# Performance work log

Measured on AMD Instinct MI355X. Metric: run time of the kernel, lower is better.

The kernel has to match this reference:

```python
import jax, jax.numpy as jnp
import numpy as np

N = 100000   # nodes
E = 1600000  # edges
G = 1000     # graphs in batch
F = 16       # in_features
D = 128      # embed_dim
C = 100      # num_centroid
K = 2        # num_class
L = 3        # num_layers


def setup_inputs() -> dict:
    key = jax.random.key(0)
    ks = jax.random.split(key, 8)
    x = jax.random.normal(ks[0], (N, F), dtype=jnp.float32)
    edge_index = jax.random.randint(ks[1], (2, E), 0, N)
    batch = jnp.sort(jax.random.randint(ks[2], (N,), 0, G))
    # learned params (xavier-like scaled, per init code)
    W_embed = jax.random.normal(ks[3], (D, F), dtype=jnp.float32) * 0.1
    W_convs = jax.random.normal(ks[4], (L, D, D), dtype=jnp.float32) * 0.05
    centroids = jax.random.normal(ks[5], (C, D), dtype=jnp.float32) * 0.1
    W_out = jax.random.normal(ks[6], (K, C), dtype=jnp.float32) * 0.1
    b_out = jax.random.uniform(ks[7], (K,), jnp.float32, -1e-4, 1e-4)
    return {"x": x, "edge_index": edge_index, "batch": batch,
            "W_embed": W_embed, "W_convs": W_convs, "centroids": centroids,
            "W_out": W_out, "b_out": b_out}


def _gcn_conv(h, W, src, dst, deg_isqrt):
    # h: [N, D]; standard GCNConv with self-loops, no bias
    m = h @ W.T                                   # [N, D]
    coef = deg_isqrt[src] * deg_isqrt[dst]        # [E+N]
    msg = m[src] * coef[:, None]                  # gather + scale
    return jax.ops.segment_sum(msg, dst, num_segments=N)


def reference(x, edge_index, batch, W_embed, W_convs, centroids, W_out, b_out):
    src0, dst0 = edge_index[0], edge_index[1]
    loop = jnp.arange(N, dtype=src0.dtype)
    src = jnp.concatenate([src0, loop])           # A + I edges
    dst = jnp.concatenate([dst0, loop])
    deg = jax.ops.segment_sum(jnp.ones(src.shape[0], jnp.float32), dst, num_segments=N)
    deg_isqrt = jax.lax.rsqrt(jnp.maximum(deg, 1.0))

    h = x @ W_embed.T                             # embedding, no bias
    for i in range(L):
        h = _gcn_conv(h, W_convs[i], src, dst, deg_isqrt)
        h = jax.nn.relu(h)                        # manifold (Euclidean) nonlinearity

    # centroid Euclidean distances: [N, C] via ||a-b||^2 = |a|^2 + |b|^2 - 2ab
    x2 = jnp.sum(h * h, axis=1, keepdims=True)            # [N,1]
    c2 = jnp.sum(centroids * centroids, axis=1)[None, :]  # [1,C]
    d2 = jnp.maximum(x2 + c2 - 2.0 * (h @ centroids.T), 0.0)
    dist = jnp.sqrt(d2 + 1e-12)                            # [N,C]

    # mean-pool per graph
    sums = jax.ops.segment_sum(dist, batch, num_segments=G)           # [G,C]
    cnts = jax.ops.segment_sum(jnp.ones((N,), jnp.float32), batch, num_segments=G)
    pooled = sums / jnp.maximum(cnts, 1.0)[:, None]

    return pooled @ W_out.T + b_out               # [G, K]
```

## Files before the change

### kernel.cpp

```cpp
#include <hip/hip_runtime.h>
#include <hip/hip_bf16.h>
#include <hip/hip_fp16.h>

constexpr int N_ = 100000;
constexpr int E_ = 1600000;
constexpr int G_ = 1000;
constexpr int D_ = 128;
constexpr int C_ = 100;
constexpr int K_ = 2;
constexpr int L_ = 3;
constexpr int NSB = (N_ + 255) / 256;
constexpr int NR_ = 8;
constexpr int RN_ = (N_ + NR_ - 1) / NR_;
constexpr int EPB_ = 1280;
constexpr int NCH_ = (E_ + EPB_ - 1) / EPB_;

using f16x8 = __attribute__((ext_vector_type(8))) _Float16;
using f16x4 = __attribute__((ext_vector_type(4))) _Float16;
using f32x4 = __attribute__((ext_vector_type(4))) float;

__global__ __launch_bounds__(256) void count_deg_xcd(
    const int* __restrict__ dstv, int* __restrict__ deg) {
    int r = blockIdx.x & 7;
    int chunk = blockIdx.x >> 3;
    int lo = r * RN_;
    int hi = lo + RN_;
    int ebeg = chunk * EPB_;
    int eend = ebeg + EPB_; if (eend > E_) eend = E_;
    for (int e = ebeg + threadIdx.x; e < eend; e += 256) {
        int d = dstv[e];
        if (d >= lo && d < hi) atomicAdd(&deg[d], 1);
    }
}

__global__ void scan_block_sums(const int* __restrict__ deg, int* __restrict__ bsums,
                                float* __restrict__ dis) {
    __shared__ int sh[256];
    int i = blockIdx.x * 256 + threadIdx.x;
    int v = (i < N_) ? deg[i] : 0;
    if (i < N_) dis[i] = 1.0f / sqrtf((float)(v + 1));
    sh[threadIdx.x] = v;
    __syncthreads();
    for (int off = 128; off > 0; off >>= 1) {
        if (threadIdx.x < off) sh[threadIdx.x] += sh[threadIdx.x + off];
        __syncthreads();
    }
    if (threadIdx.x == 0) bsums[blockIdx.x] = sh[0];
}

__global__ void scan_offsets(int* __restrict__ bsums, int nb) {
    __shared__ int a[512], b[512];
    int t = threadIdx.x;
    int v = (t < nb) ? bsums[t] : 0;
    a[t] = v;
    __syncthreads();
    int* src = a; int* dst = b;
    for (int off = 1; off < 512; off <<= 1) {
        int x = src[t] + ((t >= off) ? src[t - off] : 0);
        dst[t] = x;
        __syncthreads();
        int* tmp = src; src = dst; dst = tmp;
    }
    if (t < nb) bsums[t] = src[t] - v;
}

__global__ void scan_write(const int* __restrict__ deg, const int* __restrict__ boffs,
                           int* __restrict__ rowp) {
    __shared__ int a[256], b[256];
    int t = threadIdx.x;
    int i = blockIdx.x * 256 + t;
    int v = (i < N_) ? deg[i] : 0;
    a[t] = v;
    __syncthreads();
    int* src = a; int* dst = b;
    for (int off = 1; off < 256; off <<= 1) {
        int x = src[t] + ((t >= off) ? src[t - off] : 0);
        dst[t] = x;
        __syncthreads();
        int* tmp = src; src = dst; dst = tmp;
    }
    if (i < N_) rowp[i] = boffs[blockIdx.x] + src[t] - v;
    if (i == 0) rowp[N_] = E_;
}

__global__ __launch_bounds__(256) void fill_csr_xcd(
    const int* __restrict__ srcv, const int* __restrict__ dstv,
    const int* __restrict__ rowp, int* __restrict__ cursor,
    int* __restrict__ csr) {
    int r = blockIdx.x & 7;
    int chunk = blockIdx.x >> 3;
    int lo = r * RN_;
    int hi = lo + RN_;
    int ebeg = chunk * EPB_;
    int eend = ebeg + EPB_; if (eend > E_) eend = E_;
    for (int e = ebeg + threadIdx.x; e < eend; e += 256) {
        int d = dstv[e];
        if (d >= lo && d < hi) {
            int pos = atomicAdd(&cursor[d], 1);
            csr[rowp[d] + pos] = srcv[e];
        }
    }
}

__global__ __launch_bounds__(128) void embed_kernel(
    const float* __restrict__ x, const float* __restrict__ Wemb,
    _Float16* __restrict__ h) {
    __shared__ float4 xs[64 * 4];
    int t = threadIdx.x;
    float w[16];
#pragma unroll
    for (int f = 0; f < 16; ++f) w[f] = Wemb[t * 16 + f];
    int n0 = blockIdx.x * 64;
    const float4* x4 = (const float4*)x;
    for (int idx = t; idx < 64 * 4; idx += 128) {
        int gi = n0 * 4 + idx;
        xs[idx] = (gi < N_ * 4) ? x4[gi] : make_float4(0.f, 0.f, 0.f, 0.f);
    }
    __syncthreads();
    int lim = min(64, N_ - n0);
    for (int j = 0; j < lim; ++j) {
        float4 x0 = xs[j * 4 + 0], x1 = xs[j * 4 + 1];
        float4 x2 = xs[j * 4 + 2], x3 = xs[j * 4 + 3];
        float acc = x0.x * w[0] + x0.y * w[1] + x0.z * w[2] + x0.w * w[3]
                  + x1.x * w[4] + x1.y * w[5] + x1.z * w[6] + x1.w * w[7]
                  + x2.x * w[8] + x2.y * w[9] + x2.z * w[10] + x2.w * w[11]
                  + x3.x * w[12] + x3.y * w[13] + x3.z * w[14] + x3.w * w[15];
        h[(size_t)(n0 + j) * 128 + t] = (_Float16)acc;
    }
}

template<int FP16OUT>
__global__ __launch_bounds__(256) void mfma_gemm(
    const _Float16* __restrict__ h, const float* __restrict__ W,
    void* __restrict__ outp, int ncols, const float* __restrict__ dis) {
    int t = threadIdx.x;
    int w = t >> 6;
    int l = t & 63;
    int l15 = l & 15;
    int g = l >> 4;
    int nb0 = blockIdx.x * 128;

    f16x8 afr[2][4];
#pragma unroll
    for (int cg = 0; cg < 2; ++cg) {
        int c = 16 * w + 64 * cg + l15;
#pragma unroll
        for (int ks = 0; ks < 4; ++ks) {
            f16x8 af = {0, 0, 0, 0, 0, 0, 0, 0};
            if (c < ncols) {
                const float* wp = &W[c * 128 + 32 * ks + 8 * g];
                float4 w0 = *(const float4*)wp;
                float4 w1 = *(const float4*)(wp + 4);
                af[0] = (_Float16)w0.x; af[1] = (_Float16)w0.y;
                af[2] = (_Float16)w0.z; af[3] = (_Float16)w0.w;
                af[4] = (_Float16)w1.x; af[5] = (_Float16)w1.y;
                af[6] = (_Float16)w1.z; af[7] = (_Float16)w1.w;
            }
            afr[cg][ks] = af;
        }
    }

    for (int nt = 0; nt < 8; ++nt) {
        int nb = nb0 + 16 * nt;
        int node = nb + l15;
        int nodeL = node < N_ ? node : 0;
        f16x8 bfr[4];
#pragma unroll
        for (int ks = 0; ks < 4; ++ks)
            bfr[ks] = *(const f16x8*)&h[(size_t)nodeL * 128 + 32 * ks + 8 * g];
        f32x4 acc0 = {0.f, 0.f, 0.f, 0.f};
        f32x4 acc1 = {0.f, 0.f, 0.f, 0.f};
#pragma unroll
        for (int ks = 0; ks < 4; ++ks) {
            acc0 = __builtin_amdgcn_mfma_f32_16x16x32_f16(afr[0][ks], bfr[ks], acc0, 0, 0, 0);
            acc1 = __builtin_amdgcn_mfma_f32_16x16x32_f16(afr[1][ks], bfr[ks], acc1, 0, 0, 0);
        }
        if (node < N_) {
            int cb = 16 * w + 4 * g;
            if (FP16OUT) {
                float s = dis[node];
                ushort* mh = (ushort*)outp;
                __half2 p01 = __float22half2_rn(make_float2(acc0[0] * s, acc0[1] * s));
                __half2 p23 = __float22half2_rn(make_float2(acc0[2] * s, acc0[3] * s));
                uint2 u0;
                u0.x = *(unsigned int*)&p01; u0.y = *(unsigned int*)&p23;
                *(uint2*)&mh[(size_t)node * 128 + cb] = u0;
                __half2 q01 = __float22half2_rn(make_float2(acc1[0] * s, acc1[1] * s));
                __half2 q23 = __float22half2_rn(make_float2(acc1[2] * s, acc1[3] * s));
                uint2 u1;
                u1.x = *(unsigned int*)&q01; u1.y = *(unsigned int*)&q23;
                *(uint2*)&mh[(size_t)node * 128 + cb + 64] = u1;
            } else {
                float* o = (float*)outp;
                *(float4*)&o[(size_t)node * 128 + cb] =
                    make_float4(acc0[0], acc0[1], acc0[2], acc0[3]);
                *(float4*)&o[(size_t)node * 128 + cb + 64] =
                    make_float4(acc1[0], acc1[1], acc1[2], acc1[3]);
            }
        }
    }
}

__device__ inline float4 h4f4(uint2 u) {
    float2 fa = __half22float2(*(__half2*)&u.x);
    float2 fb = __half22float2(*(__half2*)&u.y);
    return make_float4(fa.x, fa.y, fb.x, fb.y);
}

__global__ __launch_bounds__(256) void aggregate(
    const ushort* __restrict__ mh, _Float16* __restrict__ hout,
    const int* __restrict__ rowp, const int* __restrict__ csr,
    const float* __restrict__ dis, float* __restrict__ x2out) {
    int t = threadIdx.x;
    int lane = t & 63;
    int l32 = lane & 31;
    int hbase = lane & 32;
    int node = blockIdx.x * 8 + ((t >> 6) << 1) + (hbase >> 5);
    const uint2* m2 = (const uint2*)mh;

    float4 acc0 = h4f4(m2[(size_t)node * 32 + l32]);
    float4 acc1 = make_float4(0.f, 0.f, 0.f, 0.f);
    int beg = rowp[node], end = rowp[node + 1];
    for (int base = beg; base < end; base += 32) {
        int cnt = end - base; if (cnt > 32) cnt = 32;
        int myidx = (l32 < cnt) ? csr[base + l32] : 0;
        int j = 0;
        for (; j + 8 <= cnt; j += 8) {
            int s0 = __shfl(myidx, hbase + j);
            int s1 = __shfl(myidx, hbase + j + 1);
            int s2 = __shfl(myidx, hbase + j + 2);
            int s3 = __shfl(myidx, hbase + j + 3);
            int s4 = __shfl(myidx, hbase + j + 4);
            int s5 = __shfl(myidx, hbase + j + 5);
            int s6 = __shfl(myidx, hbase + j + 6);
            int s7 = __shfl(myidx, hbase + j + 7);
            uint2 u0 = m2[(size_t)s0 * 32 + l32];
            uint2 u1 = m2[(size_t)s1 * 32 + l32];
            uint2 u2 = m2[(size_t)s2 * 32 + l32];
            uint2 u3 = m2[(size_t)s3 * 32 + l32];
            uint2 u4 = m2[(size_t)s4 * 32 + l32];
            uint2 u5 = m2[(size_t)s5 * 32 + l32];
            uint2 u6 = m2[(size_t)s6 * 32 + l32];
            uint2 u7 = m2[(size_t)s7 * 32 + l32];
            float4 v0 = h4f4(u0), v1 = h4f4(u1), v2 = h4f4(u2), v3 = h4f4(u3);
            float4 v4 = h4f4(u4), v5 = h4f4(u5), v6 = h4f4(u6), v7 = h4f4(u7);
            acc0.x += (v0.x + v1.x) + (v2.x + v3.x);
            acc0.y += (v0.y + v1.y) + (v2.y + v3.y);
            acc0.z += (v0.z + v1.z) + (v2.z + v3.z);
            acc0.w += (v0.w + v1.w) + (v2.w + v3.w);
            acc1.x += (v4.x + v5.x) + (v6.x + v7.x);
            acc1.y += (v4.y + v5.y) + (v6.y + v7.y);
            acc1.z += (v4.z + v5.z) + (v6.z + v7.z);
            acc1.w += (v4.w + v5.w) + (v6.w + v7.w);
        }
        for (; j + 4 <= cnt; j += 4) {
            int s0 = __shfl(myidx, hbase + j);
            int s1 = __shfl(myidx, hbase + j + 1);
            int s2 = __shfl(myidx, hbase + j + 2);
            int s3 = __shfl(myidx, hbase + j + 3);
            uint2 u0 = m2[(size_t)s0 * 32 + l32];
            uint2 u1 = m2[(size_t)s1 * 32 + l32];
            uint2 u2 = m2[(size_t)s2 * 32 + l32];
            uint2 u3 = m2[(size_t)s3 * 32 + l32];
            float4 v0 = h4f4(u0), v1 = h4f4(u1), v2 = h4f4(u2), v3 = h4f4(u3);
            acc0.x += (v0.x + v1.x) + (v2.x + v3.x);
            acc0.y += (v0.y + v1.y) + (v2.y + v3.y);
            acc0.z += (v0.z + v1.z) + (v2.z + v3.z);
            acc0.w += (v0.w + v1.w) + (v2.w + v3.w);
        }
        for (; j < cnt; ++j) {
            int s = __shfl(myidx, hbase + j);
            float4 v = h4f4(m2[(size_t)s * 32 + l32]);
            acc1.x += v.x; acc1.y += v.y; acc1.z += v.z; acc1.w += v.w;
        }
    }
    float di = dis[node];
    f16x4 hq;
    hq[0] = (_Float16)fmaxf(di * (acc0.x + acc1.x), 0.f);
    hq[1] = (_Float16)fmaxf(di * (acc0.y + acc1.y), 0.f);
    hq[2] = (_Float16)fmaxf(di * (acc0.z + acc1.z), 0.f);
    hq[3] = (_Float16)fmaxf(di * (acc0.w + acc1.w), 0.f);
    *(f16x4*)&hout[(size_t)node * 128 + (l32 << 2)] = hq;
    if (x2out) {
        float h0 = (float)hq[0], h1 = (float)hq[1];
        float h2 = (float)hq[2], h3 = (float)hq[3];
        float p = h0 * h0 + h1 * h1 + h2 * h2 + h3 * h3;
        p += __shfl_xor(p, 1);
        p += __shfl_xor(p, 2);
        p += __shfl_xor(p, 4);
        p += __shfl_xor(p, 8);
        p += __shfl_xor(p, 16);
        if (l32 == 0) x2out[node] = p;
    }
}

__global__ void c2_kernel(const float* __restrict__ cent, float* __restrict__ c2) {
    int c = blockIdx.x;
    int t = threadIdx.x;
    float v0 = (float)(_Float16)cent[c * 128 + t];
    float v1 = (float)(_Float16)cent[c * 128 + 64 + t];
    float p = v0 * v0 + v1 * v1;
    for (int off = 32; off > 0; off >>= 1) p += __shfl_down(p, off);
    if (t == 0) c2[c] = p;
}

__global__ __launch_bounds__(128) void pool_graph(
    const float* __restrict__ dots, const float* __restrict__ x2,
    const float* __restrict__ c2, const int* __restrict__ batch,
    float* __restrict__ pooled) {
    int g = blockIdx.x;
    int t = threadIdx.x;
    int lo = 0, hi = N_;
    while (lo < hi) { int mid = (lo + hi) >> 1; if (batch[mid] < g) lo = mid + 1; else hi = mid; }
    int s = lo;
    hi = N_;
    while (lo < hi) { int mid = (lo + hi) >> 1; if (batch[mid] < g + 1) lo = mid + 1; else hi = mid; }
    int e = lo;
    if (t >= C_) return;
    float cv = c2[t];
    float a0 = 0.f, a1 = 0.f, a2 = 0.f, a3 = 0.f;
    int n = s;
    for (; n + 4 <= e; n += 4) {
        float d0 = dots[(size_t)(n    ) * 128 + t];
        float d1 = dots[(size_t)(n + 1) * 128 + t];
        float d2 = dots[(size_t)(n + 2) * 128 + t];
        float d3 = dots[(size_t)(n + 3) * 128 + t];
        float x0 = x2[n], x1 = x2[n + 1], x2v = x2[n + 2], x3 = x2[n + 3];
        a0 += sqrtf(fmaxf(x0  + cv - 2.f * d0, 0.f) + 1e-12f);
        a1 += sqrtf(fmaxf(x1  + cv - 2.f * d1, 0.f) + 1e-12f);
        a2 += sqrtf(fmaxf(x2v + cv - 2.f * d2, 0.f) + 1e-12f);
        a3 += sqrtf(fmaxf(x3  + cv - 2.f * d3, 0.f) + 1e-12f);
    }
    for (; n < e; ++n) {
        float d = dots[(size_t)n * 128 + t];
        a0 += sqrtf(fmaxf(x2[n] + cv - 2.f * d, 0.f) + 1e-12f);
    }
    float inv = 1.0f / fmaxf((float)(e - s), 1.0f);
    pooled[g * C_ + t] = (a0 + a1 + a2 + a3) * inv;
}

__global__ void final_out(const float* __restrict__ pooled,
                          const float* __restrict__ W_out, const float* __restrict__ b_out,
                          float* __restrict__ out) {
    int i = blockIdx.x * 256 + threadIdx.x;
    if (i >= G_ * K_) return;
    int g = i >> 1, k = i & 1;
    float acc = 0.f;
    for (int c = 0; c < C_; ++c) acc += pooled[g * C_ + c] * W_out[k * C_ + c];
    out[i] = acc + b_out[k];
}

extern "C" void kernel_launch(void* const* d_in, const int* in_sizes, int n_in,
                              void* d_out, int out_size, void* d_ws, size_t ws_size,
                              hipStream_t stream) {
    const float* x       = (const float*)d_in[0];
    const int*   eidx    = (const int*)d_in[1];
    const int*   batch   = (const int*)d_in[2];
    const float* W_embed = (const float*)d_in[3];
    const float* W_convs = (const float*)d_in[4];
    const float* cent    = (const float*)d_in[5];
    const float* W_out   = (const float*)d_in[6];
    const float* b_out   = (const float*)d_in[7];
    float* out = (float*)d_out;

    char* p = (char*)d_ws;
    _Float16* h  = (_Float16*)p; p += (size_t)N_ * D_ * 2;
    float*  dots = (float*)p;  p += (size_t)N_ * D_ * 4;
    ushort* mh   = (ushort*)p; p += (size_t)N_ * D_ * 2;
    int*   deg  = (int*)p;   p += (size_t)N_ * 4;
    float* dis  = (float*)p; p += (size_t)N_ * 4;
    int*   rowp = (int*)p;   p += (size_t)(N_ + 2) * 4;
    int*   curs = (int*)p;   p += (size_t)N_ * 4;
    int*   csr  = (int*)p;   p += (size_t)E_ * 4;
    int*   bsum = (int*)p;   p += (size_t)512 * 4;
    float* c2   = (float*)p; p += (size_t)128 * 4;
    float* x2   = (float*)p; p += (size_t)N_ * 4;
    float* pool = (float*)p; p += (size_t)G_ * C_ * 4;

    const int* esrc = eidx;
    const int* edst = eidx + E_;

    hipMemsetAsync(deg, 0, (size_t)N_ * 4, stream);
    hipMemsetAsync(curs, 0, (size_t)N_ * 4, stream);

    count_deg_xcd<<<NR_ * NCH_, 256, 0, stream>>>(edst, deg);
    scan_block_sums<<<NSB, 256, 0, stream>>>(deg, bsum, dis);
    scan_offsets<<<1, 512, 0, stream>>>(bsum, NSB);
    scan_write<<<NSB, 256, 0, stream>>>(deg, bsum, rowp);
    fill_csr_xcd<<<NR_ * NCH_, 256, 0, stream>>>(esrc, edst, rowp, curs, csr);

    embed_kernel<<<(N_ + 63) / 64, 128, 0, stream>>>(x, W_embed, h);

    int ngb = (N_ + 127) / 128;
    for (int l = 0; l < L_; ++l) {
        mfma_gemm<1><<<ngb, 256, 0, stream>>>(h, W_convs + (size_t)l * D_ * D_,
                                              (void*)mh, 128, dis);
        aggregate<<<N_ / 8, 256, 0, stream>>>(mh, h, rowp, csr, dis,
                                              (l == L_ - 1) ? x2 : nullptr);
    }

    mfma_gemm<0><<<ngb, 256, 0, stream>>>(h, cent, (void*)dots, 100, nullptr);
    c2_kernel<<<C_, 64, 0, stream>>>(cent, c2);
    pool_graph<<<G_, 128, 0, stream>>>(dots, x2, c2, batch, pool);
    final_out<<<(G_ * K_ + 255) / 256, 256, 0, stream>>>(pool, W_out, b_out, out);
}
```

Baseline: 481.8 us.

## Bucket CSR neighbor lists by source-node range to improve gather locality

Splits each destination row of the CSR adjacency into 8 sub-buckets keyed by which eighth of the node range the source falls in. This needs per-(node,bucket) degree counts, an extra rowp8 offset kernel, and per-bucket cursors. The aggregate kernel then walks the buckets in order, so all waves tend to gather from the same region of the message matrix at the same time, aiming for better L2/cache hit rates. In exchange it adds two larger memsets, an extra kernel and more offset loads. It also breaks each row into tiny segments (about 2 edges per bucket), which defeats the 8-way unrolled gather loop.

```diff
diff --git a/kernel.cpp b/kernel.cpp
--- a/kernel.cpp
+++ b/kernel.cpp
@@ -11,7 +11,7 @@
 constexpr int L_ = 3;
 constexpr int NSB = (N_ + 255) / 256;
 constexpr int NR_ = 8;
-constexpr int RN_ = (N_ + NR_ - 1) / NR_;
+constexpr int RN_ = N_ / NR_;
 constexpr int EPB_ = 1280;
 constexpr int NCH_ = (E_ + EPB_ - 1) / EPB_;
 
@@ -19,8 +19,9 @@
 using f16x4 = __attribute__((ext_vector_type(4))) _Float16;
 using f32x4 = __attribute__((ext_vector_type(4))) float;
 
-__global__ __launch_bounds__(256) void count_deg_xcd(
-    const int* __restrict__ dstv, int* __restrict__ deg) {
+__global__ __launch_bounds__(256) void count_deg8_xcd(
+    const int* __restrict__ srcv, const int* __restrict__ dstv,
+    int* __restrict__ deg8) {
     int r = blockIdx.x & 7;
     int chunk = blockIdx.x >> 3;
     int lo = r * RN_;
@@ -29,16 +30,23 @@
     int eend = ebeg + EPB_; if (eend > E_) eend = E_;
     for (int e = ebeg + threadIdx.x; e < eend; e += 256) {
         int d = dstv[e];
-        if (d >= lo && d < hi) atomicAdd(&deg[d], 1);
-    }
-}
-
-__global__ void scan_block_sums(const int* __restrict__ deg, int* __restrict__ bsums,
+        if (d >= lo && d < hi) {
+            int b = srcv[e] / RN_;
+            atomicAdd(&deg8[(size_t)d * 8 + b], 1);
+        }
+    }
+}
+
+__global__ void scan_block_sums(const int* __restrict__ deg8, int* __restrict__ bsums,
                                 float* __restrict__ dis) {
     __shared__ int sh[256];
     int i = blockIdx.x * 256 + threadIdx.x;
-    int v = (i < N_) ? deg[i] : 0;
-    if (i < N_) dis[i] = 1.0f / sqrtf((float)(v + 1));
+    int v = 0;
+    if (i < N_) {
+#pragma unroll
+        for (int j = 0; j < 8; ++j) v += deg8[(size_t)i * 8 + j];
+        dis[i] = 1.0f / sqrtf((float)(v + 1));
+    }
     sh[threadIdx.x] = v;
     __syncthreads();
     for (int off = 128; off > 0; off >>= 1) {
@@ -64,12 +72,16 @@
     if (t < nb) bsums[t] = src[t] - v;
 }
 
-__global__ void scan_write(const int* __restrict__ deg, const int* __restrict__ boffs,
+__global__ void scan_write(const int* __restrict__ deg8, const int* __restrict__ boffs,
                            int* __restrict__ rowp) {
     __shared__ int a[256], b[256];
     int t = threadIdx.x;
     int i = blockIdx.x * 256 + t;
-    int v = (i < N_) ? deg[i] : 0;
+    int v = 0;
+    if (i < N_) {
+#pragma unroll
+        for (int j = 0; j < 8; ++j) v += deg8[(size_t)i * 8 + j];
+    }
     a[t] = v;
     __syncthreads();
     int* src = a; int* dst = b;
@@ -83,9 +95,26 @@
     if (i == 0) rowp[N_] = E_;
 }
 
-__global__ __launch_bounds__(256) void fill_csr_xcd(
+__global__ void build_rowp8(const int* __restrict__ deg8, const int* __restrict__ rowp,
+                            int* __restrict__ rowp8) {
+    int n = blockIdx.x * 256 + threadIdx.x;
+    if (n < N_) {
+        int base = rowp[n];
+        int o[8];
+#pragma unroll
+        for (int j = 0; j < 8; ++j) {
+            o[j] = base;
+            base += deg8[(size_t)n * 8 + j];
+        }
+#pragma unroll
+        for (int j = 0; j < 8; ++j) rowp8[(size_t)n * 8 + j] = o[j];
+    }
+    if (n == 0) rowp8[(size_t)N_ * 8] = E_;
+}
+
+__global__ __launch_bounds__(256) void fill_csr8_xcd(
     const int* __restrict__ srcv, const int* __restrict__ dstv,
-    const int* __restrict__ rowp, int* __restrict__ cursor,
+    const int* __restrict__ rowp8, int* __restrict__ cur8,
     int* __restrict__ csr) {
     int r = blockIdx.x & 7;
     int chunk = blockIdx.x >> 3;
@@ -96,8 +125,11 @@
     for (int e = ebeg + threadIdx.x; e < eend; e += 256) {
         int d = dstv[e];
         if (d >= lo && d < hi) {
-            int pos = atomicAdd(&cursor[d], 1);
-            csr[rowp[d] + pos] = srcv[e];
+            int s = srcv[e];
+            int b = s / RN_;
+            size_t idx = (size_t)d * 8 + b;
+            int pos = atomicAdd(&cur8[idx], 1);
+            csr[rowp8[idx] + pos] = s;
         }
     }
 }
@@ -207,9 +239,9 @@
     return make_float4(fa.x, fa.y, fb.x, fb.y);
 }
 
-__global__ __launch_bounds__(256) void aggregate(
+__global__ __launch_bounds__(256) void aggregate8(
     const ushort* __restrict__ mh, _Float16* __restrict__ hout,
-    const int* __restrict__ rowp, const int* __restrict__ csr,
+    const int* __restrict__ rowp8, const int* __restrict__ csr,
     const float* __restrict__ dis, float* __restrict__ x2out) {
     int t = threadIdx.x;
     int lane = t & 63;
@@ -220,58 +252,62 @@
 
     float4 acc0 = h4f4(m2[(size_t)node * 32 + l32]);
     float4 acc1 = make_float4(0.f, 0.f, 0.f, 0.f);
-    int beg = rowp[node], end = rowp[node + 1];
-    for (int base = beg; base < end; base += 32) {
-        int cnt = end - base; if (cnt > 32) cnt = 32;
-        int myidx = (l32 < cnt) ? csr[base + l32] : 0;
-        int j = 0;
-        for (; j + 8 <= cnt; j += 8) {
-            int s0 = __shfl(myidx, hbase + j);
-            int s1 = __shfl(myidx, hbase + j + 1);
-            int s2 = __shfl(myidx, hbase + j + 2);
-            int s3 = __shfl(myidx, hbase + j + 3);
-            int s4 = __shfl(myidx, hbase + j + 4);
-            int s5 = __shfl(myidx, hbase + j + 5);
-            int s6 = __shfl(myidx, hbase + j + 6);
-            int s7 = __shfl(myidx, hbase + j + 7);
-            uint2 u0 = m2[(size_t)s0 * 32 + l32];
-            uint2 u1 = m2[(size_t)s1 * 32 + l32];
-            uint2 u2 = m2[(size_t)s2 * 32 + l32];
-            uint2 u3 = m2[(size_t)s3 * 32 + l32];
-            uint2 u4 = m2[(size_t)s4 * 32 + l32];
-            uint2 u5 = m2[(size_t)s5 * 32 + l32];
-            uint2 u6 = m2[(size_t)s6 * 32 + l32];
-            uint2 u7 = m2[(size_t)s7 * 32 + l32];
-            float4 v0 = h4f4(u0), v1 = h4f4(u1), v2 = h4f4(u2), v3 = h4f4(u3);
-            float4 v4 = h4f4(u4), v5 = h4f4(u5), v6 = h4f4(u6), v7 = h4f4(u7);
-            acc0.x += (v0.x + v1.x) + (v2.x + v3.x);
-            acc0.y += (v0.y + v1.y) + (v2.y + v3.y);
-            acc0.z += (v0.z + v1.z) + (v2.z + v3.z);
-            acc0.w += (v0.w + v1.w) + (v2.w + v3.w);
-            acc1.x += (v4.x + v5.x) + (v6.x + v7.x);
-            acc1.y += (v4.y + v5.y) + (v6.y + v7.y);
-            acc1.z += (v4.z + v5.z) + (v6.z + v7.z);
-            acc1.w += (v4.w + v5.w) + (v6.w + v7.w);
-        }
-        for (; j + 4 <= cnt; j += 4) {
-            int s0 = __shfl(myidx, hbase + j);
-            int s1 = __shfl(myidx, hbase + j + 1);
-            int s2 = __shfl(myidx, hbase + j + 2);
-            int s3 = __shfl(myidx, hbase + j + 3);
-            uint2 u0 = m2[(size_t)s0 * 32 + l32];
-            uint2 u1 = m2[(size_t)s1 * 32 + l32];
-            uint2 u2 = m2[(size_t)s2 * 32 + l32];
-            uint2 u3 = m2[(size_t)s3 * 32 + l32];
-            float4 v0 = h4f4(u0), v1 = h4f4(u1), v2 = h4f4(u2), v3 = h4f4(u3);
-            acc0.x += (v0.x + v1.x) + (v2.x + v3.x);
-            acc0.y += (v0.y + v1.y) + (v2.y + v3.y);
-            acc0.z += (v0.z + v1.z) + (v2.z + v3.z);
-            acc0.w += (v0.w + v1.w) + (v2.w + v3.w);
-        }
-        for (; j < cnt; ++j) {
-            int s = __shfl(myidx, hbase + j);
-            float4 v = h4f4(m2[(size_t)s * 32 + l32]);
-            acc1.x += v.x; acc1.y += v.y; acc1.z += v.z; acc1.w += v.w;
+#pragma unroll 1
+    for (int r = 0; r < 8; ++r) {
+        int beg = rowp8[(size_t)node * 8 + r];
+        int end = rowp8[(size_t)node * 8 + r + 1];
+        for (int base = beg; base < end; base += 32) {
+            int cnt = end - base; if (cnt > 32) cnt = 32;
+            int myidx = (l32 < cnt) ? csr[base + l32] : 0;
+            int j = 0;
+            for (; j + 8 <= cnt; j += 8) {
+                int s0 = __shfl(myidx, hbase + j);
+                int s1 = __shfl(myidx, hbase + j + 1);
+                int s2 = __shfl(myidx, hbase + j + 2);
+                int s3 = __shfl(myidx, hbase + j + 3);
+                int s4 = __shfl(myidx, hbase + j + 4);
+                int s5 = __shfl(myidx, hbase + j + 5);
+                int s6 = __shfl(myidx, hbase + j + 6);
+                int s7 = __shfl(myidx, hbase + j + 7);
+                uint2 u0 = m2[(size_t)s0 * 32 + l32];
+                uint2 u1 = m2[(size_t)s1 * 32 + l32];
+                uint2 u2 = m2[(size_t)s2 * 32 + l32];
+                uint2 u3 = m2[(size_t)s3 * 32 + l32];
+                uint2 u4 = m2[(size_t)s4 * 32 + l32];
+                uint2 u5 = m2[(size_t)s5 * 32 + l32];
+                uint2 u6 = m2[(size_t)s6 * 32 + l32];
+                uint2 u7 = m2[(size_t)s7 * 32 + l32];
+                float4 v0 = h4f4(u0), v1 = h4f4(u1), v2 = h4f4(u2), v3 = h4f4(u3);
+                float4 v4 = h4f4(u4), v5 = h4f4(u5), v6 = h4f4(u6), v7 = h4f4(u7);
+                acc0.x += (v0.x + v1.x) + (v2.x + v3.x);
+                acc0.y += (v0.y + v1.y) + (v2.y + v3.y);
+                acc0.z += (v0.z + v1.z) + (v2.z + v3.z);
+                acc0.w += (v0.w + v1.w) + (v2.w + v3.w);
+                acc1.x += (v4.x + v5.x) + (v6.x + v7.x);
+                acc1.y += (v4.y + v5.y) + (v6.y + v7.y);
+                acc1.z += (v4.z + v5.z) + (v6.z + v7.z);
+                acc1.w += (v4.w + v5.w) + (v6.w + v7.w);
+            }
+            for (; j + 4 <= cnt; j += 4) {
+                int s0 = __shfl(myidx, hbase + j);
+                int s1 = __shfl(myidx, hbase + j + 1);
+                int s2 = __shfl(myidx, hbase + j + 2);
+                int s3 = __shfl(myidx, hbase + j + 3);
+                uint2 u0 = m2[(size_t)s0 * 32 + l32];
+                uint2 u1 = m2[(size_t)s1 * 32 + l32];
+                uint2 u2 = m2[(size_t)s2 * 32 + l32];
+                uint2 u3 = m2[(size_t)s3 * 32 + l32];
+                float4 v0 = h4f4(u0), v1 = h4f4(u1), v2 = h4f4(u2), v3 = h4f4(u3);
+                acc0.x += (v0.x + v1.x) + (v2.x + v3.x);
+                acc0.y += (v0.y + v1.y) + (v2.y + v3.y);
+                acc0.z += (v0.z + v1.z) + (v2.z + v3.z);
+                acc0.w += (v0.w + v1.w) + (v2.w + v3.w);
+            }
+            for (; j < cnt; ++j) {
+                int s = __shfl(myidx, hbase + j);
+                float4 v = h4f4(m2[(size_t)s * 32 + l32]);
+                acc1.x += v.x; acc1.y += v.y; acc1.z += v.z; acc1.w += v.w;
+            }
         }
     }
     float di = dis[node];
@@ -367,10 +403,11 @@
     _Float16* h  = (_Float16*)p; p += (size_t)N_ * D_ * 2;
     float*  dots = (float*)p;  p += (size_t)N_ * D_ * 4;
     ushort* mh   = (ushort*)p; p += (size_t)N_ * D_ * 2;
-    int*   deg  = (int*)p;   p += (size_t)N_ * 4;
+    int*   deg8 = (int*)p;   p += (size_t)N_ * 8 * 4;
+    int*   cur8 = (int*)p;   p += (size_t)N_ * 8 * 4;
+    int*   rowp8= (int*)p;   p += ((size_t)N_ * 8 + 2) * 4;
     float* dis  = (float*)p; p += (size_t)N_ * 4;
     int*   rowp = (int*)p;   p += (size_t)(N_ + 2) * 4;
-    int*   curs = (int*)p;   p += (size_t)N_ * 4;
     int*   csr  = (int*)p;   p += (size_t)E_ * 4;
     int*   bsum = (int*)p;   p += (size_t)512 * 4;
     float* c2   = (float*)p; p += (size_t)128 * 4;
@@ -380,14 +417,15 @@
     const int* esrc = eidx;
     const int* edst = eidx + E_;
 
-    hipMemsetAsync(deg, 0, (size_t)N_ * 4, stream);
-    hipMemsetAsync(curs, 0, (size_t)N_ * 4, stream);
-
-    count_deg_xcd<<<NR_ * NCH_, 256, 0, stream>>>(edst, deg);
-    scan_block_sums<<<NSB, 256, 0, stream>>>(deg, bsum, dis);
+    hipMemsetAsync(deg8, 0, (size_t)N_ * 8 * 4, stream);
+    hipMemsetAsync(cur8, 0, (size_t)N_ * 8 * 4, stream);
+
+    count_deg8_xcd<<<NR_ * NCH_, 256, 0, stream>>>(esrc, edst, deg8);
+    scan_block_sums<<<NSB, 256, 0, stream>>>(deg8, bsum, dis);
     scan_offsets<<<1, 512, 0, stream>>>(bsum, NSB);
-    scan_write<<<NSB, 256, 0, stream>>>(deg, bsum, rowp);
-    fill_csr_xcd<<<NR_ * NCH_, 256, 0, stream>>>(esrc, edst, rowp, curs, csr);
+    scan_write<<<NSB, 256, 0, stream>>>(deg8, bsum, rowp);
+    build_rowp8<<<NSB, 256, 0, stream>>>(deg8, rowp, rowp8);
+    fill_csr8_xcd<<<NR_ * NCH_, 256, 0, stream>>>(esrc, edst, rowp8, cur8, csr);
 
     embed_kernel<<<(N_ + 63) / 64, 128, 0, stream>>>(x, W_embed, h);
 
@@ -395,8 +433,8 @@
     for (int l = 0; l < L_; ++l) {
         mfma_gemm<1><<<ngb, 256, 0, stream>>>(h, W_convs + (size_t)l * D_ * D_,
                                               (void*)mh, 128, dis);
-        aggregate<<<N_ / 8, 256, 0, stream>>>(mh, h, rowp, csr, dis,
-                                              (l == L_ - 1) ? x2 : nullptr);
+        aggregate8<<<N_ / 8, 256, 0, stream>>>(mh, h, rowp8, csr, dis,
+                                               (l == L_ - 1) ? x2 : nullptr);
     }
 
     mfma_gemm<0><<<ngb, 256, 0, stream>>>(h, cent, (void*)dots, 100, nullptr);
```

New measurement: 610.6 us. +26.7%, slower.
